# Optimization experiments

Measured on AMD Instinct MI355X. Metric: run time of the kernel, lower is better.

## Reference

```python
import jax, jax.numpy as jnp
import numpy as np

N_NODES = 32000
N_EDGES = 512000
F_IN = 128
HEADS = 4
CH = 64
NODES_PER_GRAPH = 500
BATCH = 64
HID = 512
ZDIM = 64


def _gat_layer(x, src, dst, W, att_src, att_dst, bias):
    # PyG GATConv, concat=True, negative_slope=0.2, self-loops already appended.
    N = x.shape[0]
    h = (x @ W).reshape(N, HEADS, CH)                 # [N,H,C]
    a_s = jnp.sum(h * att_src, axis=-1)               # [N,H]
    a_d = jnp.sum(h * att_dst, axis=-1)               # [N,H]
    e = jax.nn.leaky_relu(a_s[src] + a_d[dst], negative_slope=0.2)  # [E,H]
    m = jax.ops.segment_max(e, dst, num_segments=N)   # segment softmax over dst
    p = jnp.exp(e - m[dst])
    denom = jax.ops.segment_sum(p, dst, num_segments=N)
    alpha = p / denom[dst]                            # [E,H]
    out = jax.ops.segment_sum(h[src] * alpha[..., None], dst, num_segments=N)
    return out.reshape(N, HEADS * CH) + bias


def setup_inputs() -> dict:
    key = jax.random.key(0)
    ks = jax.random.split(key, 16)
    s = 0.02
    x = jax.random.normal(ks[0], (N_NODES, F_IN), jnp.float32)
    edge_index = jax.random.randint(ks[1], (2, N_EDGES), 0, N_NODES, jnp.int64)
    W1 = jax.random.normal(ks[2], (F_IN, HEADS * CH), jnp.float32) * s
    att_src1 = jax.random.normal(ks[3], (HEADS, CH), jnp.float32) * s
    att_dst1 = jax.random.normal(ks[4], (HEADS, CH), jnp.float32) * s
    b1 = jnp.zeros((HEADS * CH,), jnp.float32)
    W2 = jax.random.normal(ks[5], (HEADS * CH, HEADS * CH), jnp.float32) * s
    att_src2 = jax.random.normal(ks[6], (HEADS, CH), jnp.float32) * s
    att_dst2 = jax.random.normal(ks[7], (HEADS, CH), jnp.float32) * s
    b2 = jnp.zeros((HEADS * CH,), jnp.float32)
    We = jax.random.normal(ks[8], (NODES_PER_GRAPH * HEADS * CH, HID), jnp.float32) * 0.002
    be = jnp.zeros((HID,), jnp.float32)
    Wmu = jax.random.normal(ks[9], (HID, ZDIM), jnp.float32) * s
    bmu = jnp.zeros((ZDIM,), jnp.float32)
    Wvar = jax.random.normal(ks[10], (HID, ZDIM), jnp.float32) * s
    bvar = jnp.zeros((ZDIM,), jnp.float32)
    return {"x": x, "W1": W1, "att_src1": att_src1, "att_dst1": att_dst1, "b1": b1,
            "W2": W2, "att_src2": att_src2, "att_dst2": att_dst2, "b2": b2,
            "We": We, "be": be, "Wmu": Wmu, "bmu": bmu, "Wvar": Wvar, "bvar": bvar,
            "edge_index": edge_index, "batch": BATCH}


def reference(x, W1, att_src1, att_dst1, b1, W2, att_src2, att_dst2, b2,
              We, be, Wmu, bmu, Wvar, bvar, edge_index, batch):
    N = x.shape[0]
    loops = jnp.arange(N, dtype=edge_index.dtype)
    src = jnp.concatenate([edge_index[0], loops])
    dst = jnp.concatenate([edge_index[1], loops])
    h = jax.nn.relu(_gat_layer(x, src, dst, W1, att_src1, att_dst1, b1))
    h = jax.nn.relu(_gat_layer(h, src, dst, W2, att_src2, att_dst2, b2))
    xg = h.reshape(batch, -1)                         # [B, in_fea*H*C]
    y = xg @ We + be                                  # [B, HID]
    mu_b = jnp.mean(y, axis=0)                        # BatchNorm1d (training stats), eps=1e-3
    var_b = jnp.var(y, axis=0)
    y = (y - mu_b) / jnp.sqrt(var_b + 1e-3)
    mu_l = jnp.mean(y, axis=-1, keepdims=True)        # LayerNorm, no affine, eps=1e-5
    var_l = jnp.var(y, axis=-1, keepdims=True)
    y = (y - mu_l) / jnp.sqrt(var_l + 1e-5)
    y = jax.nn.relu(y)
    z_loc = y @ Wmu + bmu
    z_scale = jnp.exp(y @ Wvar + bvar) + 1e-4
    return (z_loc, z_scale)
```

## Files before the change

### kernel.cpp

```cpp
#include <hip/hip_runtime.h>
#include <math.h>

#define NN 32000
#define FIN 128
#define HC 256
#define NH 4
#define HIDD 512
#define BB 64
#define ZD 64
#define NSPLIT 250
#define KBCH 512
#define BNB 128

typedef __bf16 bf16x8 __attribute__((ext_vector_type(8)));
typedef float f32x4 __attribute__((ext_vector_type(4)));
typedef unsigned int uint;

__device__ inline float lrelu(float x){ return x > 0.f ? x : 0.2f*x; }
__device__ inline unsigned short f2b(float f){
  uint u = __float_as_uint(f);
  return (unsigned short)((u + 0x7FFFu + ((u >> 16) & 1u)) >> 16);
}
__device__ inline float b2f(unsigned short b){ return __uint_as_float(((uint)b) << 16); }
__device__ inline float blo(uint v){ return __uint_as_float(v << 16); }
__device__ inline float bhi(uint v){ return __uint_as_float(v & 0xffff0000u); }
__device__ inline uint cvtpk(float lo, float hi){
  uint pk;
  asm("v_cvt_pk_bf16_f32 %0, %1, %2" : "=v"(pk) : "v"(lo), "v"(hi));
  return pk;
}

__global__ void k_prep0(const void* ei, int* flag, int* counts){
  int b = blockIdx.x, t = threadIdx.x;
  if (b == 0 && t < 64){
    int v = ((const int*)ei)[2*t + 1];
    unsigned long long bal = __ballot(v == 0);
    if (t == 0) *flag = (bal == ~0ULL) ? 1 : 0;
  }
  for (int i = b*256 + t; i < NN; i += gridDim.x*256) counts[i] = 0;
}

__global__ void k_prep1(const float* __restrict__ x, unsigned short* __restrict__ xb,
                        const float* __restrict__ W1, unsigned short* __restrict__ Wt1,
                        const float* __restrict__ W2, unsigned short* __restrict__ Wt2,
                        const void* ei, const int* __restrict__ flag,
                        int* __restrict__ counts, int E){
  int b = blockIdx.x, t = threadIdx.x;
  if (b < 16000){
    int i = b*256 + t;
    xb[i] = f2b(x[i]);
  } else if (b < 16512){
    int bb = b - 16000;
    int n = bb & 255, which = bb >> 8;
    if (which == 0){ if (t < FIN) Wt1[n*FIN + t] = f2b(W1[t*HC + n]); }
    else           { Wt2[n*HC + t] = f2b(W2[t*HC + n]); }
  } else {
    int i = (b - 16512)*256 + t;
    if (i < E){
      int d = *flag ? (int)((const long long*)ei)[E + i] : ((const int*)ei)[E + i];
      atomicAdd(&counts[d], 1);
    }
  }
}

__global__ __launch_bounds__(1024) void k_scan(const int* __restrict__ counts,
    int* __restrict__ offs, int* __restrict__ cursor, int n){
  __shared__ int sums[1024];
  int t = threadIdx.x;
  const int CHK = 32;
  int base = t * CHK;
  int s = 0;
  for (int i = 0; i < CHK; i++){ int idx = base + i; if (idx < n) s += counts[idx]; }
  sums[t] = s;
  __syncthreads();
  for (int off = 1; off < 1024; off <<= 1){
    int v = (t >= off) ? sums[t - off] : 0;
    __syncthreads();
    sums[t] += v;
    __syncthreads();
  }
  int run = (t == 0) ? 0 : sums[t-1];
  for (int i = 0; i < CHK; i++){
    int idx = base + i;
    if (idx < n){ offs[idx] = run; cursor[idx] = run; run += counts[idx]; }
  }
  if (t == 1023) offs[n] = sums[1023];
}

__global__ void k_fill(const void* ei, const int* __restrict__ flag,
                       int* __restrict__ cursor, int* __restrict__ col, int E){
  int i = blockIdx.x*256 + threadIdx.x;
  if (i < E){
    int s, d;
    if (*flag){ s = (int)((const long long*)ei)[i]; d = (int)((const long long*)ei)[E + i]; }
    else      { s = ((const int*)ei)[i];            d = ((const int*)ei)[E + i]; }
    int pos = atomicAdd(&cursor[d], 1);
    col[pos] = s;
  }
}

__global__ __launch_bounds__(256) void k_gemm_n(const unsigned short* __restrict__ A,
    const unsigned short* __restrict__ Wt, int K,
    const float* __restrict__ ws, const float* __restrict__ wd,
    unsigned short* __restrict__ out, float* __restrict__ a_s, float* __restrict__ a_d){
  __shared__ unsigned short As[64][40];
  __shared__ unsigned short Bs[256][40];
  int m0 = blockIdx.x * 64;
  int t = threadIdx.x;
  int w = t >> 6, lane = t & 63, l15 = lane & 15, l16 = lane >> 4;
  f32x4 acc[16];
  #pragma unroll
  for (int c = 0; c < 16; c++) acc[c] = (f32x4){0.f,0.f,0.f,0.f};

  for (int k0 = 0; k0 < K; k0 += 32){
    {
      int row = t >> 2, ko = (t & 3) * 8;
      *(uint4*)&As[row][ko] = *(const uint4*)&A[(size_t)(m0 + row)*K + k0 + ko];
    }
    {
      #pragma unroll
      for (int p = 0; p < 4; p++)
        *(uint4*)&Bs[t][p*8] = *(const uint4*)&Wt[(size_t)t*K + k0 + p*8];
    }
    __syncthreads();
    bf16x8 af = *(const bf16x8*)&As[w*16 + l15][l16*8];
    #pragma unroll
    for (int c = 0; c < 16; c++){
      bf16x8 bfr = *(const bf16x8*)&Bs[c*16 + l15][l16*8];
      acc[c] = __builtin_amdgcn_mfma_f32_16x16x32_bf16(af, bfr, acc[c], 0, 0, 0);
    }
    __syncthreads();
  }

  #pragma unroll
  for (int r = 0; r < 4; r++){
    int row = m0 + w*16 + l16*4 + r;
    float hs[NH] = {0,0,0,0}, hd[NH] = {0,0,0,0};
    #pragma unroll
    for (int c = 0; c < 16; c++){
      float v = acc[c][r];
      int colc = c*16 + l15;
      out[(size_t)row*HC + colc] = f2b(v);
      hs[c>>2] += v * ws[colc];
      hd[c>>2] += v * wd[colc];
    }
    #pragma unroll
    for (int h = 0; h < NH; h++){
      float s = hs[h], d = hd[h];
      #pragma unroll
      for (int o = 1; o < 16; o <<= 1){ s += __shfl_xor(s, o); d += __shfl_xor(d, o); }
      if (l15 == h){ a_s[row*NH + h] = s; a_d[row*NH + h] = d; }
    }
  }
}

__global__ __launch_bounds__(256) void k_agg(const unsigned short* __restrict__ hp,
    const int* __restrict__ col, const int* __restrict__ offs,
    const float* __restrict__ a_s, const float* __restrict__ a_d,
    const float* __restrict__ bias, unsigned short* __restrict__ outb){
  int n = blockIdx.x*4 + (threadIdx.x >> 6);
  int lane = threadIdx.x & 63;
  int g = lane >> 4, l16 = lane & 15;
  int h = l16 >> 2;
  int c0 = l16 * 16;
  int b0 = offs[n], b1 = offs[n+1];
  float adh = a_d[n*NH + h];
  float pself = expf(lrelu(a_s[n*NH + h] + adh));
  float den = 0.f;
  float ac[16];
  #pragma unroll
  for (int j = 0; j < 16; j++) ac[j] = 0.f;
  #pragma unroll 2
  for (int i = b0 + g; i < b1; i += 4){
    int s = col[i];
    float p = expf(lrelu(a_s[s*NH + h] + adh));
    den += p;
    uint4 v0 = *(const uint4*)&hp[(size_t)s*HC + c0];
    uint4 v1 = *(const uint4*)&hp[(size_t)s*HC + c0 + 8];
    ac[0] = fmaf(p, blo(v0.x), ac[0]);   ac[1] = fmaf(p, bhi(v0.x), ac[1]);
    ac[2] = fmaf(p, blo(v0.y), ac[2]);   ac[3] = fmaf(p, bhi(v0.y), ac[3]);
    ac[4] = fmaf(p, blo(v0.z), ac[4]);   ac[5] = fmaf(p, bhi(v0.z), ac[5]);
    ac[6] = fmaf(p, blo(v0.w), ac[6]);   ac[7] = fmaf(p, bhi(v0.w), ac[7]);
    ac[8] = fmaf(p, blo(v1.x), ac[8]);   ac[9] = fmaf(p, bhi(v1.x), ac[9]);
    ac[10]= fmaf(p, blo(v1.y), ac[10]);  ac[11]= fmaf(p, bhi(v1.y), ac[11]);
    ac[12]= fmaf(p, blo(v1.z), ac[12]);  ac[13]= fmaf(p, bhi(v1.z), ac[13]);
    ac[14]= fmaf(p, blo(v1.w), ac[14]);  ac[15]= fmaf(p, bhi(v1.w), ac[15]);
  }
  den += __shfl_xor(den, 16);  den += __shfl_xor(den, 32);
  #pragma unroll
  for (int j = 0; j < 16; j++){
    ac[j] += __shfl_xor(ac[j], 16);
    ac[j] += __shfl_xor(ac[j], 32);
  }
  den += pself;
  float r = 1.f / den;
  if (g == 0){
    uint4 hv0 = *(const uint4*)&hp[(size_t)n*HC + c0];
    uint4 hv1 = *(const uint4*)&hp[(size_t)n*HC + c0 + 8];
    float hvf[16] = {blo(hv0.x),bhi(hv0.x),blo(hv0.y),bhi(hv0.y),
                     blo(hv0.z),bhi(hv0.z),blo(hv0.w),bhi(hv0.w),
                     blo(hv1.x),bhi(hv1.x),blo(hv1.y),bhi(hv1.y),
                     blo(hv1.z),bhi(hv1.z),blo(hv1.w),bhi(hv1.w)};
    uint ov[8];
    #pragma unroll
    for (int j = 0; j < 8; j++){
      float e0 = fmaxf((pself*hvf[2*j]   + ac[2*j]  )*r + bias[c0+2*j],   0.f);
      float e1 = fmaxf((pself*hvf[2*j+1] + ac[2*j+1])*r + bias[c0+2*j+1], 0.f);
      ov[j] = ((uint)f2b(e1) << 16) | (uint)f2b(e0);
    }
    *(uint4*)&outb[(size_t)n*HC + c0]     = *(uint4*)&ov[0];
    *(uint4*)&outb[(size_t)n*HC + c0 + 8] = *(uint4*)&ov[4];
  }
}

__global__ __launch_bounds__(256) void k_gemm_big(const unsigned short* __restrict__ xg,
    const float* __restrict__ We, float* __restrict__ part){
  __shared__ unsigned short As[2][64][40];
  __shared__ unsigned short Bs[2][BNB][40];
  int n0 = blockIdx.x * BNB;
  int kc = blockIdx.y;
  int kbase = kc * KBCH;
  int t = threadIdx.x, w = t >> 6, lane = t & 63, l15 = lane & 15, l16 = lane >> 4;
  int cc = t & (BNB-1);
  int khalf = t >> 7;
  int arow = t >> 2, ako = (t & 3) * 8;
  const float* bptr = We + (size_t)(kbase + khalf*16)*HIDD + n0 + cc;
  const unsigned short* aptr = xg + (size_t)arow*128000 + kbase + ako;
  f32x4 acc[8];
  #pragma unroll
  for (int c = 0; c < 8; c++) acc[c] = (f32x4){0.f,0.f,0.f,0.f};

  float rv[16]; uint4 a4;
  #pragma unroll
  for (int mm = 0; mm < 16; mm++) rv[mm] = bptr[(size_t)mm*HIDD];
  a4 = *(const uint4*)aptr;

  int p = 0;
  for (int ks = 0; ks < KBCH; ks += 32){
    *(uint4*)&As[p][arow][ako] = a4;
    #pragma unroll
    for (int j = 0; j < 8; j++)
      *(uint*)&Bs[p][cc][khalf*16 + 2*j] = cvtpk(rv[2*j], rv[2*j+1]);
    __syncthreads();
    if (ks + 32 < KBCH){
      const float* bp2 = bptr + (size_t)(ks + 32)*HIDD;
      #pragma unroll
      for (int mm = 0; mm < 16; mm++) rv[mm] = bp2[(size_t)mm*HIDD];
      a4 = *(const uint4*)(aptr + ks + 32);
    }
    bf16x8 af = *(const bf16x8*)&As[p][w*16 + l15][l16*8];
    #pragma unroll
    for (int c = 0; c < 8; c++){
      bf16x8 bfr = *(const bf16x8*)&Bs[p][c*16 + l15][l16*8];
      acc[c] = __builtin_amdgcn_mfma_f32_16x16x32_bf16(af, bfr, acc[c], 0, 0, 0);
    }
    p ^= 1;
  }
  float* pbase = part + (size_t)kc*BB*HIDD;
  #pragma unroll
  for (int r = 0; r < 4; r++){
    int row = w*16 + l16*4 + r;
    #pragma unroll
    for (int c = 0; c < 8; c++)
      pbase[row*HIDD + n0 + c*16 + l15] = acc[c][r];
  }
}

__global__ void k_reduce(const float* __restrict__ part, const float* __restrict__ be,
                         float* __restrict__ y){
  int o = blockIdx.x*256 + threadIdx.x;
  float s = 0.f;
  #pragma unroll 5
  for (int k = 0; k < NSPLIT; k++) s += part[(size_t)k*BB*HIDD + o];
  y[o] = s + be[o & (HIDD-1)];
}

__global__ __launch_bounds__(64) void k_bn(const float* __restrict__ y,
    float* __restrict__ ybn){
  int colb = blockIdx.x, r = threadIdx.x;
  float v = y[(size_t)r*HIDD + colb];
  float s = v, s2 = v*v;
  #pragma unroll
  for (int o = 32; o; o >>= 1){ s += __shfl_down(s, o); s2 += __shfl_down(s2, o); }
  s = __shfl(s, 0); s2 = __shfl(s2, 0);
  float mean = s * (1.f/BB);
  float var = s2 * (1.f/BB) - mean*mean;
  ybn[(size_t)r*HIDD + colb] = (v - mean) * rsqrtf(var + 1e-3f);
}

__global__ __launch_bounds__(512) void k_lnheads(const float* __restrict__ ybn,
    const float* __restrict__ Wmu, const float* __restrict__ bmu,
    const float* __restrict__ Wvar, const float* __restrict__ bvar,
    float* __restrict__ out){
  __shared__ float ssum[8], ssq[8];
  __shared__ float yrow[HIDD];
  int row = blockIdx.x, t = threadIdx.x;
  float v = ybn[(size_t)row*HIDD + t];
  float s = v, s2 = v*v;
  #pragma unroll
  for (int o = 32; o; o >>= 1){ s += __shfl_down(s, o); s2 += __shfl_down(s2, o); }
  if ((t & 63) == 0){ ssum[t>>6] = s; ssq[t>>6] = s2; }
  __syncthreads();
  if (t == 0){
    float S = 0, S2 = 0;
    for (int i = 0; i < 8; i++){ S += ssum[i]; S2 += ssq[i]; }
    ssum[0] = S; ssq[0] = S2;
  }
  __syncthreads();
  float mean = ssum[0] * (1.f/HIDD);
  float var = ssq[0] * (1.f/HIDD) - mean*mean;
  yrow[t] = fmaxf((v - mean) * rsqrtf(var + 1e-5f), 0.f);
  __syncthreads();
  int o = t >> 2, kq = t & 3;
  const float* Wc = (o < ZD) ? Wmu : Wvar;
  int j = (o < ZD) ? o : o - ZD;
  float acc = 0.f;
  #pragma unroll 4
  for (int k = kq*128; k < kq*128 + 128; k++)
    acc = fmaf(yrow[k], Wc[(size_t)k*ZD + j], acc);
  acc += __shfl_down(acc, 1);
  acc += __shfl_down(acc, 2);
  if (kq == 0){
    if (o < ZD) out[row*ZD + o] = acc + bmu[o];
    else        out[BB*ZD + row*ZD + j] = expf(acc + bvar[j]) + 1e-4f;
  }
}

extern "C" void kernel_launch(void* const* d_in, const int* in_sizes, int n_in,
                              void* d_out, int out_size, void* d_ws, size_t ws_size,
                              hipStream_t stream){
  const float* x    = (const float*)d_in[0];
  const float* W1   = (const float*)d_in[1];
  const float* as1  = (const float*)d_in[2];
  const float* ad1  = (const float*)d_in[3];
  const float* b1   = (const float*)d_in[4];
  const float* W2   = (const float*)d_in[5];
  const float* as2  = (const float*)d_in[6];
  const float* ad2  = (const float*)d_in[7];
  const float* b2   = (const float*)d_in[8];
  const float* We   = (const float*)d_in[9];
  const float* be   = (const float*)d_in[10];
  const float* Wmu  = (const float*)d_in[11];
  const float* bmu  = (const float*)d_in[12];
  const float* Wvar = (const float*)d_in[13];
  const float* bvar = (const float*)d_in[14];
  const void*  ei   = d_in[15];
  int E = in_sizes[15] / 2;

  char* w = (char*)d_ws;
  auto alloc = [&](size_t bytes)->void*{
    void* p = (void*)w; w += (bytes + 255) & ~(size_t)255; return p;
  };
  unsigned short* gb   = (unsigned short*)alloc((size_t)NN*HC*2);
  unsigned short* ab   = (unsigned short*)alloc((size_t)NN*HC*2);
  unsigned short* xb   = (unsigned short*)alloc((size_t)NN*FIN*2);
  unsigned short* Wt1  = (unsigned short*)alloc((size_t)HC*FIN*2);
  unsigned short* Wt2  = (unsigned short*)alloc((size_t)HC*HC*2);
  float*    a_s    = (float*)alloc((size_t)NN*NH*4);
  float*    a_d    = (float*)alloc((size_t)NN*NH*4);
  int*      counts = (int*)alloc((size_t)NN*4);
  int*      offs   = (int*)alloc((size_t)(NN+1)*4);
  int*      cursor = (int*)alloc((size_t)NN*4);
  int*      col    = (int*)alloc((size_t)E*4);
  int*      flag   = (int*)alloc(256);
  float*    part   = (float*)alloc((size_t)NSPLIT*BB*HIDD*4);
  float*    y      = (float*)alloc((size_t)BB*HIDD*4);
  float*    ybn    = (float*)alloc((size_t)BB*HIDD*4);

  k_prep0<<<125, 256, 0, stream>>>(ei, flag, counts);
  k_prep1<<<16512 + (E + 255)/256, 256, 0, stream>>>(x, xb, W1, Wt1, W2, Wt2,
                                                     ei, flag, counts, E);
  k_scan<<<1, 1024, 0, stream>>>(counts, offs, cursor, NN);
  k_fill<<<(E + 255)/256, 256, 0, stream>>>(ei, flag, cursor, col, E);

  k_gemm_n<<<NN/64, 256, 0, stream>>>(xb, Wt1, FIN, as1, ad1, gb, a_s, a_d);
  k_agg<<<NN/4, 256, 0, stream>>>(gb, col, offs, a_s, a_d, b1, ab);

  k_gemm_n<<<NN/64, 256, 0, stream>>>(ab, Wt2, HC, as2, ad2, gb, a_s, a_d);
  k_agg<<<NN/4, 256, 0, stream>>>(gb, col, offs, a_s, a_d, b2, ab);

  k_gemm_big<<<dim3(HIDD/BNB, NSPLIT), 256, 0, stream>>>(ab, We, part);
  k_reduce<<<BB*HIDD/256, 256, 0, stream>>>(part, be, y);
  k_bn<<<HIDD, 64, 0, stream>>>(y, ybn);
  k_lnheads<<<BB, 512, 0, stream>>>(ybn, Wmu, bmu, Wvar, bvar, (float*)d_out);
}
```

Before: 356.2 us.

## Replace single-block prefix scan with three-pass multi-block scan

The single 1024-thread block scan over the 32000 degree counts is replaced by a reduce-then-scan scheme: per-block sums over 125 blocks, a small scan of the block sums, then per-block exclusive scans plus the block offset. This spreads the scan over many CUs instead of one serial-chunked block with uncoalesced strided reads. It adds two extra kernel launches, which may offset the gain since the original scan was small.

```diff
diff --git a/kernel.cpp b/kernel.cpp
--- a/kernel.cpp
+++ b/kernel.cpp
@@ -63,28 +63,52 @@
   }
 }
 
-__global__ __launch_bounds__(1024) void k_scan(const int* __restrict__ counts,
-    int* __restrict__ offs, int* __restrict__ cursor, int n){
-  __shared__ int sums[1024];
+__global__ __launch_bounds__(256) void k_scanA(const int* __restrict__ counts,
+                                               int* __restrict__ bsum){
+  __shared__ int red[256];
+  int b = blockIdx.x, t = threadIdx.x;
+  red[t] = counts[b*256 + t];
+  __syncthreads();
+  #pragma unroll
+  for (int o = 128; o; o >>= 1){
+    if (t < o) red[t] += red[t + o];
+    __syncthreads();
+  }
+  if (t == 0) bsum[b] = red[0];
+}
+
+__global__ __launch_bounds__(128) void k_scanB(int* __restrict__ bsum, int nb){
+  __shared__ int s[128];
   int t = threadIdx.x;
-  const int CHK = 32;
-  int base = t * CHK;
-  int s = 0;
-  for (int i = 0; i < CHK; i++){ int idx = base + i; if (idx < n) s += counts[idx]; }
-  sums[t] = s;
-  __syncthreads();
-  for (int off = 1; off < 1024; off <<= 1){
-    int v = (t >= off) ? sums[t - off] : 0;
-    __syncthreads();
-    sums[t] += v;
-    __syncthreads();
-  }
-  int run = (t == 0) ? 0 : sums[t-1];
-  for (int i = 0; i < CHK; i++){
-    int idx = base + i;
-    if (idx < n){ offs[idx] = run; cursor[idx] = run; run += counts[idx]; }
-  }
-  if (t == 1023) offs[n] = sums[1023];
+  int v = (t < nb) ? bsum[t] : 0;
+  s[t] = v;
+  __syncthreads();
+  for (int o = 1; o < 128; o <<= 1){
+    int u = (t >= o) ? s[t - o] : 0;
+    __syncthreads();
+    s[t] += u;
+    __syncthreads();
+  }
+  if (t < nb) bsum[t] = s[t] - v;
+}
+
+__global__ __launch_bounds__(256) void k_scanC(const int* __restrict__ counts,
+    const int* __restrict__ bsum, int* __restrict__ offs, int* __restrict__ cursor){
+  __shared__ int s[256];
+  int b = blockIdx.x, t = threadIdx.x;
+  int v = counts[b*256 + t];
+  s[t] = v;
+  __syncthreads();
+  for (int o = 1; o < 256; o <<= 1){
+    int u = (t >= o) ? s[t - o] : 0;
+    __syncthreads();
+    s[t] += u;
+    __syncthreads();
+  }
+  int excl = s[t] - v + bsum[b];
+  offs[b*256 + t] = excl;
+  cursor[b*256 + t] = excl;
+  if (b == (NN/256 - 1) && t == 255) offs[NN] = excl + v;
 }
 
 __global__ void k_fill(const void* ei, const int* __restrict__ flag,
@@ -362,6 +386,7 @@
   int*      offs   = (int*)alloc((size_t)(NN+1)*4);
   int*      cursor = (int*)alloc((size_t)NN*4);
   int*      col    = (int*)alloc((size_t)E*4);
+  int*      bsum   = (int*)alloc((size_t)256*4);
   int*      flag   = (int*)alloc(256);
   float*    part   = (float*)alloc((size_t)NSPLIT*BB*HIDD*4);
   float*    y      = (float*)alloc((size_t)BB*HIDD*4);
@@ -370,7 +395,9 @@
   k_prep0<<<125, 256, 0, stream>>>(ei, flag, counts);
   k_prep1<<<16512 + (E + 255)/256, 256, 0, stream>>>(x, xb, W1, Wt1, W2, Wt2,
                                                      ei, flag, counts, E);
-  k_scan<<<1, 1024, 0, stream>>>(counts, offs, cursor, NN);
+  k_scanA<<<NN/256, 256, 0, stream>>>(counts, bsum);
+  k_scanB<<<1, 128, 0, stream>>>(bsum, NN/256);
+  k_scanC<<<NN/256, 256, 0, stream>>>(counts, bsum, offs, cursor);
   k_fill<<<(E + 255)/256, 256, 0, stream>>>(ei, flag, cursor, col, E);
 
   k_gemm_n<<<NN/64, 256, 0, stream>>>(xb, Wt1, FIN, as1, ad1, gb, a_s, a_d);
```

Result: faster. 289.4 us (-18.8%).
